# Optimization experiments

Measured on AMD Instinct MI355X. Metric: run time of the kernel, lower is better.

## Reference

```python
import jax, jax.numpy as jnp
import numpy as np

B, P, NTIME, NLATENT, NSPATIAL = 4, 2, 16, 32, 2048


def sqrt_act(x):
    # signed square root: sign(x) * sqrt(|x|) (odd, monotone activation used in ERA5_PredRNN)
    return jnp.sign(x) * jnp.sqrt(jnp.abs(x))


def setup_inputs() -> dict:
    key = jax.random.key(0)
    ks = jax.random.split(key, 10)
    T, C, X = NTIME, NLATENT, NSPATIAL
    # xavier-uniform bounds (torch fan_in = T*C, fan_out = T*C for (t,T,c); T,T for 2D)
    s3 = (6.0 / (T * C + T * C)) ** 0.5
    s2 = (6.0 / (T + T)) ** 0.5
    x = jax.random.normal(ks[0], (B, P, T, C, X), jnp.float32)
    K0 = jax.random.uniform(ks[1], (T, T, C), jnp.float32, -s3, s3)
    Q0 = jax.random.uniform(ks[2], (T, T, C), jnp.float32, -s3, s3)
    V0 = jax.random.uniform(ks[3], (T, T, C), jnp.float32, -s3, s3)
    K1 = jax.random.uniform(ks[4], (T, T), jnp.float32, -s2, s2)
    Q1 = jax.random.uniform(ks[5], (T, T), jnp.float32, -s2, s2)
    V1 = jax.random.uniform(ks[6], (T, T), jnp.float32, -s2, s2)

    def ortho3(kk):
        # mimics nn.init.orthogonal_ on (T,T,T): rows (flattened to T x T*T) are orthonormal
        m = jax.random.normal(kk, (T * T, T), jnp.float32)
        q, _ = jnp.linalg.qr(m)  # (T*T, T), orthonormal columns
        return q.T.reshape(T, T, T)

    enc = ortho3(ks[7])
    dec = ortho3(ks[8])
    a = jnp.ones((T, X), jnp.float32)
    w = jnp.ones((T, X), jnp.float32) / (X * T)
    return dict(x=x, K0=K0, Q0=Q0, V0=V0, K1=K1, Q1=Q1, V1=V1,
                enc=enc, dec=dec, a=a, w=w)


def reference(x, K0, Q0, V0, K1, Q1, V1, enc, dec, a, w):
    # --- layer 0: per-latent-channel time mixing (tTc) ---
    k = jnp.einsum('tTc,bpTcx->bptcx', K0, x)
    q0 = jnp.einsum('tTc,bpTcx->bptcx', Q0, x)
    v = jnp.einsum('tTc,bpTcx->bptcx', V0, x)
    h = sqrt_act(jnp.einsum('bptcx,bpTcx,etT->bpecx', k, v, enc))
    # --- layer 1: shared time mixing (tT) ---
    k = jnp.einsum('tT,bpTcx->bptcx', K1, h)
    q1 = jnp.einsum('tT,bpTcx->bptcx', Q1, h)
    v = jnp.einsum('tT,bpTcx->bptcx', V1, h)
    h = sqrt_act(jnp.einsum('bptcx,bpTcx,etT->bpecx', k, v, enc))
    # estp: 'tx,bptcx->bptcx' (elementwise over t,x)
    b = a[None, None, :, None, :] * h
    # decoder mixing in reverse layer order (estb)
    b = jnp.einsum('bptcx,bpecx,etT->bpTcx', q1, b, dec)
    b = jnp.einsum('bptcx,bpecx,etT->bpTcx', q0, b, dec)
    # estc: 'tx,bptcx->bpc'
    y = jnp.einsum('tx,bptcx->bpc', w, b)
    return y[:, :, None, :]  # [B, p, 1, c]
```

## Files before the change

kernel.cpp:

```cpp
#include <hip/hip_runtime.h>
#include <math.h>

#define NB 4
#define NP 2
#define NT 16
#define NC 32
#define NX 2048
#define HS 20


typedef _Float16 f16x8 __attribute__((ext_vector_type(8)));
typedef float f32x16 __attribute__((ext_vector_type(16)));

__device__ __forceinline__ unsigned short f16hi_bits(float v) {
    _Float16 h = (_Float16)v;
    return __builtin_bit_cast(unsigned short, h);
}
__device__ __forceinline__ unsigned short f16lo_bits(float v) {
    _Float16 h = (_Float16)v;
    _Float16 l = (_Float16)(v - (float)h);
    return __builtin_bit_cast(unsigned short, l);
}
__device__ __forceinline__ f16x8 frag_cast(uint4 u) {
    return __builtin_bit_cast(f16x8, u);
}
__device__ __forceinline__ float sqrt_act(float v) {
    return copysignf(sqrtf(fabsf(v)), v);
}
__device__ __forceinline__ f32x16 zero16() {
    f32x16 z;
#pragma unroll
    for (int i = 0; i < 16; ++i) z[i] = 0.f;
    return z;
}

__device__ void g_compute(const float* __restrict__ K,
                          const float* __restrict__ V,
                          const float* __restrict__ enc,
                          int cstride, int c, int e, int tid,
                          float* sK, float* sV, float* sE, float* sW,
                          float* outG) {
    {
        const int t = tid >> 4, A = tid & 15;
        sK[tid] = K[(t * 16 + A) * cstride + c];
        sV[tid] = V[(t * 16 + A) * cstride + c];
        sE[tid] = enc[(e * 16 + t) * 16 + A];
    }
    __syncthreads();
    {
        const int t = tid >> 4, Bi = tid & 15;
        float acc = 0.f;
#pragma unroll
        for (int T = 0; T < 16; ++T) acc += sE[t * 16 + T] * sV[T * 16 + Bi];
        sW[tid] = acc;
    }
    __syncthreads();
    {
        const int A = tid >> 4, Bi = tid & 15;
        float acc = 0.f;
#pragma unroll
        for (int t = 0; t < 16; ++t) acc += sK[t * 16 + A] * sW[t * 16 + Bi];
        outG[tid] = acc;
    }
    __syncthreads();
}

__device__ void emit_pair(const float* sGa, const float* sGb,
                          uint4* __restrict__ dst, int tid) {
    if (tid < 128) {
        const int part = tid >> 6, lane = tid & 63;
        const int row32 = lane & 31, g = lane >> 5;
        const float* src = (row32 & 16) ? sGb : sGa;
        const int row = row32 & 15;
        unsigned dw[4];
#pragma unroll
        for (int d = 0; d < 4; ++d) {
            const float v0 = src[row * 16 + g * 8 + 2 * d];
            const float v1 = src[row * 16 + g * 8 + 2 * d + 1];
            const unsigned short s0 = part ? f16lo_bits(v0) : f16hi_bits(v0);
            const unsigned short s1 = part ? f16lo_bits(v1) : f16hi_bits(v1);
            dw[d] = (unsigned)s0 | ((unsigned)s1 << 16);
        }
        dst[part * 64 + lane] = make_uint4(dw[0], dw[1], dw[2], dw[3]);
    }
}

__global__ __launch_bounds__(256) void precompute_all(
    const float* __restrict__ K0, const float* __restrict__ V0,
    const float* __restrict__ K1, const float* __restrict__ V1,
    const float* __restrict__ Q0, const float* __restrict__ Q1,
    const float* __restrict__ enc, const float* __restrict__ dec,
    uint4* __restrict__ AF0, uint4* __restrict__ AFG1,
    uint4* __restrict__ AFM1, uint4* __restrict__ AFM2) {
    __shared__ float sK[256], sV[256], sE[256], sW[256], sGa[256], sGb[256];
    const int b = blockIdx.x, tid = threadIdx.x;
    if (b < 256) {
        const int c = b >> 3, m = b & 7;
        g_compute(K0, V0, enc, NC, c, 2 * m,     tid, sK, sV, sE, sW, sGa);
        g_compute(K0, V0, enc, NC, c, 2 * m + 1, tid, sK, sV, sE, sW, sGb);
        emit_pair(sGa, sGb, AF0 + (c * 8 + m) * 128, tid);
    } else if (b < 264) {
        const int m = b - 256;
        g_compute(K1, V1, enc, 1, 0, 2 * m,     tid, sK, sV, sE, sW, sGa);
        g_compute(K1, V1, enc, 1, 0, 2 * m + 1, tid, sK, sV, sE, sW, sGb);
        emit_pair(sGa, sGb, AFG1 + m * 128, tid);
    } else if (b < 272) {
        const int m = b - 264;
        if (tid < 128) {
            const int part = tid >> 6, lane = tid & 63;
            const int row32 = lane & 31, g = lane >> 5;
            const int e = 2 * m + (row32 >> 4), E = row32 & 15;
            unsigned dw[4];
#pragma unroll
            for (int d = 0; d < 4; ++d) {
                unsigned short s01[2];
#pragma unroll
                for (int hh = 0; hh < 2; ++hh) {
                    const int T = g * 8 + 2 * d + hh;
                    float acc = 0.f;
#pragma unroll
                    for (int t = 0; t < 16; ++t)
                        acc += Q1[t * 16 + T] * dec[(e * 16 + t) * 16 + E];
                    s01[hh] = part ? f16lo_bits(acc) : f16hi_bits(acc);
                }
                dw[d] = (unsigned)s01[0] | ((unsigned)s01[1] << 16);
            }
            AFM1[m * 128 + part * 64 + lane] = make_uint4(dw[0], dw[1], dw[2], dw[3]);
        }
    } else if (b < 528) {
        const int idx = b - 272;
        const int c = idx >> 3, m = idx & 7;
        if (tid < 128) {
            const int part = tid >> 6, lane = tid & 63;
            const int row32 = lane & 31, g = lane >> 5;
            const int T = 2 * m + (row32 >> 4), A = row32 & 15;
            unsigned dw[4];
#pragma unroll
            for (int d = 0; d < 4; ++d) {
                unsigned short s01[2];
#pragma unroll
                for (int hh = 0; hh < 2; ++hh) {
                    const int E = g * 8 + 2 * d + hh;
                    float acc = 0.f;
#pragma unroll
                    for (int t = 0; t < 16; ++t)
                        acc += Q0[(t * 16 + A) * NC + c] * dec[(E * 16 + t) * 16 + T];
                    s01[hh] = part ? f16lo_bits(acc) : f16hi_bits(acc);
                }
                dw[d] = (unsigned)s01[0] | ((unsigned)s01[1] << 16);
            }
            AFM2[(c * 8 + m) * 128 + part * 64 + lane] =
                make_uint4(dw[0], dw[1], dw[2], dw[3]);
        }
    } else {
        if (tid < 128) AFM2[256 * 128 + tid] = make_uint4(0u, 0u, 0u, 0u);
    }
}

__global__ __launch_bounds__(256) void site_kernel(
    const float* __restrict__ x,
    const float* __restrict__ a,
    const float* __restrict__ w,
    const uint4* __restrict__ AF0,
    const uint4* __restrict__ AFG1,
    const uint4* __restrict__ AFM1,
    const uint4* __restrict__ AFM2,
    float* __restrict__ out) {
    __shared__ float hlds[4][32 * HS];
    __shared__ float red[4];

    const int tid = threadIdx.x;
    const int lane = tid & 63, wid = tid >> 6;
    const int col = lane & 31, g = lane >> 5;
    const int bid = blockIdx.x;
    const int xg = bid & 15;
    const int c  = (bid >> 4) & 31;
    const int bp = bid >> 9;
    const int xA = xg * 128 + wid * 32 + col;
    const float* xb = x + (bp * NT * NC + c) * NX;
    float* hl = hlds[wid];

    f16x8 Xh, Xl;
    float XC[8];
#pragma unroll
    for (int j = 0; j < 8; ++j) {
        const float v = xb[(g * 8 + j) * NC * NX + xA];
        const _Float16 h = (_Float16)v;
        Xh[j] = h; Xl[j] = (_Float16)(v - (float)h);
    }
#pragma unroll
    for (int r = 0; r < 8; ++r) {
        const int A = (r & 3) + 8 * (r >> 2) + 4 * g;
        XC[r] = xb[A * NC * NX + xA];
    }

    {
        const uint4* p0 = AF0 + (c * 8) * 128;
#pragma unroll 1
        for (int m = 0; m < 8; ++m) {
            const f16x8 Ah = frag_cast(p0[lane]);
            const f16x8 Al = frag_cast(p0[64 + lane]);
            p0 += 128;
            f32x16 C = zero16();
            C = __builtin_amdgcn_mfma_f32_32x32x16_f16(Ah, Xh, C, 0, 0, 0);
            C = __builtin_amdgcn_mfma_f32_32x32x16_f16(Ah, Xl, C, 0, 0, 0);
            C = __builtin_amdgcn_mfma_f32_32x32x16_f16(Al, Xh, C, 0, 0, 0);
            C = __builtin_amdgcn_mfma_f32_32x32x16_f16(Al, Xl, C, 0, 0, 0);
            float se = 0.f, so = 0.f;
#pragma unroll
            for (int r = 0; r < 8; ++r) {
                se += XC[r] * C[r];
                so += XC[r] * C[r + 8];
            }
            se += __shfl_xor(se, 32);
            so += __shfl_xor(so, 32);
            hl[col * HS + 2 * m]     = sqrt_act(se);
            hl[col * HS + 2 * m + 1] = sqrt_act(so);
        }
    }

    f16x8 hH, hL;
    float hC[8];
#pragma unroll
    for (int j = 0; j < 8; ++j) {
        const float v = hl[col * HS + g * 8 + j];
        const _Float16 h = (_Float16)v;
        hH[j] = h; hL[j] = (_Float16)(v - (float)h);
    }
#pragma unroll
    for (int r = 0; r < 8; ++r)
        hC[r] = hl[col * HS + (r & 3) + 8 * (r >> 2) + 4 * g];

    float b2[8];
#pragma unroll
    for (int r = 0; r < 8; ++r) b2[r] = 0.f;
    {
        const uint4* pG = AFG1;
        const uint4* pM = AFM1;
        const float* pa = a + xA;
#pragma unroll 1
        for (int m = 0; m < 8; ++m) {
            const f16x8 GH = frag_cast(pG[lane]);
            const f16x8 GL = frag_cast(pG[64 + lane]);
            const f16x8 MH = frag_cast(pM[lane]);
            const f16x8 ML = frag_cast(pM[64 + lane]);
            pG += 128; pM += 128;
            const float ae = pa[0], ao = pa[NX];
            pa += 2 * NX;
            f32x16 C = zero16();
            C = __builtin_amdgcn_mfma_f32_32x32x16_f16(GH, hH, C, 0, 0, 0);
            C = __builtin_amdgcn_mfma_f32_32x32x16_f16(GH, hL, C, 0, 0, 0);
            C = __builtin_amdgcn_mfma_f32_32x32x16_f16(GL, hH, C, 0, 0, 0);
            C = __builtin_amdgcn_mfma_f32_32x32x16_f16(GL, hL, C, 0, 0, 0);
            float se = 0.f, so = 0.f;
#pragma unroll
            for (int r = 0; r < 8; ++r) {
                se += hC[r] * C[r];
                so += hC[r] * C[r + 8];
            }
            se += __shfl_xor(se, 32);
            so += __shfl_xor(so, 32);
            const float pe = ae * sqrt_act(se);
            const float po = ao * sqrt_act(so);
            f32x16 U = zero16();
            U = __builtin_amdgcn_mfma_f32_32x32x16_f16(MH, hH, U, 0, 0, 0);
            U = __builtin_amdgcn_mfma_f32_32x32x16_f16(MH, hL, U, 0, 0, 0);
            U = __builtin_amdgcn_mfma_f32_32x32x16_f16(ML, hH, U, 0, 0, 0);
            U = __builtin_amdgcn_mfma_f32_32x32x16_f16(ML, hL, U, 0, 0, 0);
#pragma unroll
            for (int r = 0; r < 8; ++r)
                b2[r] += pe * U[r] + po * U[r + 8];
        }
    }

#pragma unroll
    for (int r = 0; r < 4; ++r) {
        hl[col * HS + r + 4 * g]     = b2[r];
        hl[col * HS + 8 + r + 4 * g] = b2[r + 4];
    }
    f16x8 bH, bL;
#pragma unroll
    for (int j = 0; j < 8; ++j) {
        const float v = hl[col * HS + g * 8 + j];
        const _Float16 h = (_Float16)v;
        bH[j] = h; bL[j] = (_Float16)(v - (float)h);
    }

    float ya = 0.f;
    {
        const uint4* p2 = AFM2 + (c * 8) * 128;
        const float* pw = w + xA;
#pragma unroll 1
        for (int m = 0; m < 8; ++m) {
            const f16x8 MH = frag_cast(p2[lane]);
            const f16x8 ML = frag_cast(p2[64 + lane]);
            p2 += 128;
            const float we = pw[0], wo = pw[NX];
            pw += 2 * NX;
            f32x16 Z = zero16();
            Z = __builtin_amdgcn_mfma_f32_32x32x16_f16(MH, bH, Z, 0, 0, 0);
            Z = __builtin_amdgcn_mfma_f32_32x32x16_f16(MH, bL, Z, 0, 0, 0);
            Z = __builtin_amdgcn_mfma_f32_32x32x16_f16(ML, bH, Z, 0, 0, 0);
            Z = __builtin_amdgcn_mfma_f32_32x32x16_f16(ML, bL, Z, 0, 0, 0);
            float se = 0.f, so = 0.f;
#pragma unroll
            for (int r = 0; r < 8; ++r) {
                se += XC[r] * Z[r];
                so += XC[r] * Z[r + 8];
            }
            ya += we * se + wo * so;
        }
    }

    float y = ya + __shfl_xor(ya, 32);
    y += __shfl_xor(y, 1); y += __shfl_xor(y, 2);
    y += __shfl_xor(y, 4); y += __shfl_xor(y, 8); y += __shfl_xor(y, 16);
    if (lane == 0) red[wid] = y;
    __syncthreads();
    if (tid == 0) {
        atomicAdd(&out[bp * NC + c], red[0] + red[1] + red[2] + red[3]);
    }
}

extern "C" void kernel_launch(void* const* d_in, const int* in_sizes, int n_in,
                              void* d_out, int out_size, void* d_ws, size_t ws_size,
                              hipStream_t stream) {
    const float* x   = (const float*)d_in[0];
    const float* K0  = (const float*)d_in[1];
    const float* Q0  = (const float*)d_in[2];
    const float* V0  = (const float*)d_in[3];
    const float* K1  = (const float*)d_in[4];
    const float* Q1  = (const float*)d_in[5];
    const float* V1  = (const float*)d_in[6];
    const float* enc = (const float*)d_in[7];
    const float* dec = (const float*)d_in[8];
    const float* a   = (const float*)d_in[9];
    const float* w   = (const float*)d_in[10];
    float* out = (float*)d_out;

    uint4* AF0  = (uint4*)d_ws;
    uint4* AFG1 = AF0  + 256 * 128;
    uint4* AFM1 = AFG1 + 8 * 128;
    uint4* AFM2 = AFM1 + 8 * 128;

    hipMemsetAsync(d_out, 0, (size_t)out_size * sizeof(float), stream);

    precompute_all<<<529, 256, 0, stream>>>(K0, V0, K1, V1, Q0, Q1,
                                            enc, dec, AF0, AFG1, AFM1, AFM2);

    const int nblocks = NB * NP * NC * (NX / 128);
    site_kernel<<<nblocks, 256, 0, stream>>>(x, a, w, AF0, AFG1, AFM1, AFM2, out);
}
```

Before: 179.8 us.

## Drop lo*lo MFMA terms, split precompute per e, fold output zeroing

Removes the low-times-low MFMA product from each split-f16 product in every stage of the site kernel, cutting the matrix work per fragment from four MFMAs to three. The precompute kernel now computes one encoder slice per block instead of two, so it runs more blocks, each with a shorter serial chain. Output zeroing moves into the last precompute block, which removes the separate memset launch. Dropping the lo*lo term lowers accuracy slightly; its contribution is normally far below the fp32 tolerance.

```diff
diff --git a/kernel.cpp b/kernel.cpp
--- a/kernel.cpp
+++ b/kernel.cpp
@@ -65,23 +65,21 @@
     __syncthreads();
 }
 
-__device__ void emit_pair(const float* sGa, const float* sGb,
-                          uint4* __restrict__ dst, int tid) {
-    if (tid < 128) {
-        const int part = tid >> 6, lane = tid & 63;
-        const int row32 = lane & 31, g = lane >> 5;
-        const float* src = (row32 & 16) ? sGb : sGa;
-        const int row = row32 & 15;
+__device__ void emit_half(const float* sG, uint4* __restrict__ dstPair,
+                          int half, int tid) {
+    if (tid < 64) {
+        const int row = tid & 15, g = (tid >> 4) & 1, part = tid >> 5;
         unsigned dw[4];
 #pragma unroll
         for (int d = 0; d < 4; ++d) {
-            const float v0 = src[row * 16 + g * 8 + 2 * d];
-            const float v1 = src[row * 16 + g * 8 + 2 * d + 1];
+            const float v0 = sG[row * 16 + g * 8 + 2 * d];
+            const float v1 = sG[row * 16 + g * 8 + 2 * d + 1];
             const unsigned short s0 = part ? f16lo_bits(v0) : f16hi_bits(v0);
             const unsigned short s1 = part ? f16lo_bits(v1) : f16hi_bits(v1);
             dw[d] = (unsigned)s0 | ((unsigned)s1 << 16);
         }
-        dst[part * 64 + lane] = make_uint4(dw[0], dw[1], dw[2], dw[3]);
+        dstPair[part * 64 + g * 32 + 16 * half + row] =
+            make_uint4(dw[0], dw[1], dw[2], dw[3]);
     }
 }
 
@@ -91,21 +89,20 @@
     const float* __restrict__ Q0, const float* __restrict__ Q1,
     const float* __restrict__ enc, const float* __restrict__ dec,
     uint4* __restrict__ AF0, uint4* __restrict__ AFG1,
-    uint4* __restrict__ AFM1, uint4* __restrict__ AFM2) {
-    __shared__ float sK[256], sV[256], sE[256], sW[256], sGa[256], sGb[256];
+    uint4* __restrict__ AFM1, uint4* __restrict__ AFM2,
+    float* __restrict__ out) {
+    __shared__ float sK[256], sV[256], sE[256], sW[256], sG[256];
     const int b = blockIdx.x, tid = threadIdx.x;
-    if (b < 256) {
-        const int c = b >> 3, m = b & 7;
-        g_compute(K0, V0, enc, NC, c, 2 * m,     tid, sK, sV, sE, sW, sGa);
-        g_compute(K0, V0, enc, NC, c, 2 * m + 1, tid, sK, sV, sE, sW, sGb);
-        emit_pair(sGa, sGb, AF0 + (c * 8 + m) * 128, tid);
-    } else if (b < 264) {
-        const int m = b - 256;
-        g_compute(K1, V1, enc, 1, 0, 2 * m,     tid, sK, sV, sE, sW, sGa);
-        g_compute(K1, V1, enc, 1, 0, 2 * m + 1, tid, sK, sV, sE, sW, sGb);
-        emit_pair(sGa, sGb, AFG1 + m * 128, tid);
-    } else if (b < 272) {
-        const int m = b - 264;
+    if (b < 512) {
+        const int c = b >> 4, e = b & 15;
+        g_compute(K0, V0, enc, NC, c, e, tid, sK, sV, sE, sW, sG);
+        emit_half(sG, AF0 + (c * 8 + (e >> 1)) * 128, e & 1, tid);
+    } else if (b < 528) {
+        const int e = b - 512;
+        g_compute(K1, V1, enc, 1, 0, e, tid, sK, sV, sE, sW, sG);
+        emit_half(sG, AFG1 + (e >> 1) * 128, e & 1, tid);
+    } else if (b < 536) {
+        const int m = b - 528;
         if (tid < 128) {
             const int part = tid >> 6, lane = tid & 63;
             const int row32 = lane & 31, g = lane >> 5;
@@ -127,8 +124,8 @@
             }
             AFM1[m * 128 + part * 64 + lane] = make_uint4(dw[0], dw[1], dw[2], dw[3]);
         }
-    } else if (b < 528) {
-        const int idx = b - 272;
+    } else if (b < 792) {
+        const int idx = b - 536;
         const int c = idx >> 3, m = idx & 7;
         if (tid < 128) {
             const int part = tid >> 6, lane = tid & 63;
@@ -154,6 +151,7 @@
         }
     } else {
         if (tid < 128) AFM2[256 * 128 + tid] = make_uint4(0u, 0u, 0u, 0u);
+        out[tid] = 0.f;
     }
 }
 
@@ -205,7 +203,6 @@
             C = __builtin_amdgcn_mfma_f32_32x32x16_f16(Ah, Xh, C, 0, 0, 0);
             C = __builtin_amdgcn_mfma_f32_32x32x16_f16(Ah, Xl, C, 0, 0, 0);
             C = __builtin_amdgcn_mfma_f32_32x32x16_f16(Al, Xh, C, 0, 0, 0);
-            C = __builtin_amdgcn_mfma_f32_32x32x16_f16(Al, Xl, C, 0, 0, 0);
             float se = 0.f, so = 0.f;
 #pragma unroll
             for (int r = 0; r < 8; ++r) {
@@ -251,7 +248,6 @@
             C = __builtin_amdgcn_mfma_f32_32x32x16_f16(GH, hH, C, 0, 0, 0);
             C = __builtin_amdgcn_mfma_f32_32x32x16_f16(GH, hL, C, 0, 0, 0);
             C = __builtin_amdgcn_mfma_f32_32x32x16_f16(GL, hH, C, 0, 0, 0);
-            C = __builtin_amdgcn_mfma_f32_32x32x16_f16(GL, hL, C, 0, 0, 0);
             float se = 0.f, so = 0.f;
 #pragma unroll
             for (int r = 0; r < 8; ++r) {
@@ -266,7 +262,6 @@
             U = __builtin_amdgcn_mfma_f32_32x32x16_f16(MH, hH, U, 0, 0, 0);
             U = __builtin_amdgcn_mfma_f32_32x32x16_f16(MH, hL, U, 0, 0, 0);
             U = __builtin_amdgcn_mfma_f32_32x32x16_f16(ML, hH, U, 0, 0, 0);
-            U = __builtin_amdgcn_mfma_f32_32x32x16_f16(ML, hL, U, 0, 0, 0);
 #pragma unroll
             for (int r = 0; r < 8; ++r)
                 b2[r] += pe * U[r] + po * U[r + 8];
@@ -301,7 +296,6 @@
             Z = __builtin_amdgcn_mfma_f32_32x32x16_f16(MH, bH, Z, 0, 0, 0);
             Z = __builtin_amdgcn_mfma_f32_32x32x16_f16(MH, bL, Z, 0, 0, 0);
             Z = __builtin_amdgcn_mfma_f32_32x32x16_f16(ML, bH, Z, 0, 0, 0);
-            Z = __builtin_amdgcn_mfma_f32_32x32x16_f16(ML, bL, Z, 0, 0, 0);
             float se = 0.f, so = 0.f;
 #pragma unroll
             for (int r = 0; r < 8; ++r) {
@@ -343,10 +337,9 @@
     uint4* AFM1 = AFG1 + 8 * 128;
     uint4* AFM2 = AFM1 + 8 * 128;
 
-    hipMemsetAsync(d_out, 0, (size_t)out_size * sizeof(float), stream);
-
-    precompute_all<<<529, 256, 0, stream>>>(K0, V0, K1, V1, Q0, Q1,
-                                            enc, dec, AF0, AFG1, AFM1, AFM2);
+    precompute_all<<<793, 256, 0, stream>>>(K0, V0, K1, V1, Q0, Q1,
+                                            enc, dec, AF0, AFG1, AFM1, AFM2,
+                                            out);
 
     const int nblocks = NB * NP * NC * (NX / 128);
     site_kernel<<<nblocks, 256, 0, stream>>>(x, a, w, AF0, AFG1, AFM1, AFM2, out);
```

Result: faster. 168.4 us (-6.4%).
